# Kernel tuning notes

Hardware: AMD Instinct MI355X
Metric: run time of the kernel (lower is better)

Reference implementation:

```python
import jax, jax.numpy as jnp
import numpy as np

N, K, D, H, DK, DV, L, E = 16384, 16, 128, 8, 16, 16, 2, 32
DFF = 4 * D
EPS = 1e-5


def _ln(x, g, b):
    mu = jnp.mean(x, axis=-1, keepdims=True)
    var = jnp.var(x, axis=-1, keepdims=True)
    return (x - mu) * jax.lax.rsqrt(var + EPS) * g + b


def setup_inputs() -> dict:
    key = jax.random.key(0)
    ks = jax.random.split(key, 20)
    inp = {
        "node_h": jax.random.normal(ks[0], (N, D), jnp.float32),
        "src_idx": jax.random.randint(ks[1], (N, K), 0, N),
        "edge_feat": jax.random.normal(ks[2], (N, K, E), jnp.float32),
        "t": jax.random.uniform(ks[3], (N, K), jnp.float32),
        "t_now": jnp.ones((1,), jnp.float32),
        # params (linear weights stored [in, out])
        "edge_fc_w": jax.random.normal(ks[4], (E, D), jnp.float32) * (2.0 / (E + D)) ** 0.5,
        "edge_fc_b": jnp.zeros((D,), jnp.float32),
        "basis_freq": jnp.asarray(1.0 / 10 ** np.linspace(0, 9, D), jnp.float32),
        "phase": jax.random.normal(ks[5], (D,), jnp.float32),
        "wq": jax.random.normal(ks[6], (L, D, H * DK), jnp.float32) * np.sqrt(2.0 / (D + DK)),
        "wk": jax.random.normal(ks[7], (L, D, H * DK), jnp.float32) * np.sqrt(2.0 / (D + DK)),
        "wv": jax.random.normal(ks[8], (L, D, H * DV), jnp.float32) * np.sqrt(2.0 / (D + DV)),
        "attn_fc_w": jax.random.normal(ks[9], (L, H * DV, D), jnp.float32) * (2.0 / (H * DV + D)) ** 0.5,
        "attn_fc_b": jnp.zeros((L, D), jnp.float32),
        "attn_ln_g": jnp.ones((L, D), jnp.float32),
        "attn_ln_b": jnp.zeros((L, D), jnp.float32),
        "ffn_w1": jax.random.normal(ks[10], (L, D, DFF), jnp.float32) * (1.0 / D) ** 0.5,
        "ffn_b1": jnp.zeros((L, DFF), jnp.float32),
        "ffn_w2": jax.random.normal(ks[11], (L, DFF, D), jnp.float32) * (1.0 / DFF) ** 0.5,
        "ffn_b2": jnp.zeros((L, D), jnp.float32),
        "ffn_ln_g": jnp.ones((L, D), jnp.float32),
        "ffn_ln_b": jnp.zeros((L, D), jnp.float32),
        "fea2node_w": jax.random.normal(ks[12], (D, D), jnp.float32) * (2.0 / (D + D)) ** 0.5,
        "fea2node_b": jnp.zeros((D,), jnp.float32),
        "final_ln_g": jnp.ones((D,), jnp.float32),
        "final_ln_b": jnp.zeros((D,), jnp.float32),
    }
    return inp


def reference(node_h, src_idx, edge_feat, t, t_now,
              edge_fc_w, edge_fc_b, basis_freq, phase,
              wq, wk, wv, attn_fc_w, attn_fc_b, attn_ln_g, attn_ln_b,
              ffn_w1, ffn_b1, ffn_w2, ffn_b2, ffn_ln_g, ffn_ln_b,
              fea2node_w, fea2node_b, final_ln_g, final_ln_b):
    scale = 1.0 / np.sqrt(DK).astype(np.float32)
    # message_func: gather src features, edge transform, temporal encoding
    t_enc = jnp.cos((t_now[0] - t)[..., None] * basis_freq + phase)        # [N,K,D]
    z = node_h[src_idx] + jax.nn.gelu(edge_feat @ edge_fc_w + edge_fc_b) + t_enc
    # reduce_func: inner_layer transformer blocks over the K-neighbor mailbox
    f = z
    for i in range(L):
        q = (f @ wq[i]).reshape(N, K, H, DK)
        k = (f @ wk[i]).reshape(N, K, H, DK)
        v = (f @ wv[i]).reshape(N, K, H, DV)
        attn = jax.nn.softmax(jnp.einsum('nqhd,nkhd->nhqk', q, k) * scale, axis=-1)
        out = jnp.einsum('nhqk,nkhd->nqhd', attn, v).reshape(N, K, H * DV)
        f = _ln(out @ attn_fc_w[i] + attn_fc_b[i] + f, attn_ln_g[i], attn_ln_b[i])
        hid = jax.nn.relu(f @ ffn_w1[i] + ffn_b1[i])                        # [N,K,4D]
        f = _ln(hid @ ffn_w2[i] + ffn_b2[i] + f, ffn_ln_g[i], ffn_ln_b[i])
    pooled = jnp.mean(f, axis=1)                                            # [N,D]
    out = _ln(jax.nn.gelu(pooled @ fea2node_w + fea2node_b) + node_h,
              final_ln_g, final_ln_b)
    return out
```

## Files before the change

### kernel.cpp

```cpp
#include <hip/hip_runtime.h>

#define NN 16384
#define OFF_EWT 0
#define OFF_WQT 4096
#define OFF_WKT 36864
#define OFF_WVT 69632
#define OFF_AFT 102400
#define OFF_W1T 135168
#define OFF_W2T 266240
#define OFF_F2N 397312
#define TOTAL_W 413696
#define FB_BYTE_OFF (1 << 20)

typedef __attribute__((ext_vector_type(8))) short bf16x8;
typedef __attribute__((ext_vector_type(4))) short bf16x4;
typedef __attribute__((ext_vector_type(4))) float f32x4;

static __device__ __forceinline__ short f2bf(float f) {
  unsigned u = __builtin_bit_cast(unsigned, f);
  u += 0x7fffu + ((u >> 16) & 1u);
  return (short)(u >> 16);
}
static __device__ __forceinline__ float bf2f(short h) {
  unsigned u = ((unsigned)(unsigned short)h) << 16;
  return __builtin_bit_cast(float, u);
}
static __device__ __forceinline__ float gelu_f(float x) {
  float e = __expf(1.5957691216057308f * (x + 0.044715f * x * x * x));
  return x - x / (e + 1.0f);
}
static __device__ __forceinline__ f32x4 mfma16(bf16x8 a, bf16x8 b, f32x4 c) {
  return __builtin_amdgcn_mfma_f32_16x16x32_bf16(a, b, c, 0, 0, 0);
}
#define SWZM(row) (((((row) & 7) << 4)) ^ ((((row) >> 3) & 3) << 5))
static __device__ __forceinline__ int swzb(int row, int col) {
  return row * 256 + ((col * 2) ^ SWZM(row));
}
static __device__ __forceinline__ bf16x8 tile_ld8(const short* base, int row, int col) {
  return *(const bf16x8*)((const char*)base + swzb(row, col));
}
static __device__ __forceinline__ void tile_st16(short* base, int row, int col, short v) {
  *(short*)((char*)base + swzb(row, col)) = v;
}
static __device__ __forceinline__ float tile_ldf(const short* base, int row, int col) {
  return bf2f(*(const short*)((const char*)base + swzb(row, col)));
}
static __device__ __forceinline__ void gll16(const short* sp, void* dstb) {
  __builtin_amdgcn_global_load_lds(
      (const __attribute__((address_space(1))) unsigned int*)sp,
      (__attribute__((address_space(3))) unsigned int*)dstb, 16, 0, 0);
}
static __device__ __forceinline__ void stage_h8(short* dst, const short* src, int stride,
                                                int w, int lane) {
  #pragma unroll
  for (int it = 0; it < 2; ++it) {
    int dbase = (it * 8 + w) * 1024;
    int d = dbase + lane * 16;
    int row = d >> 8;
    int scolb = (d & 255) ^ SWZM(row);
    gll16(src + row * stride + (scolb >> 1), (char*)dst + dbase);
  }
}
static __device__ __forceinline__ void stage_full8(short* dst, const short* src, int stride,
                                                   int w, int lane) {
  #pragma unroll
  for (int it = 0; it < 4; ++it) {
    int dbase = (it * 8 + w) * 1024;
    int d = dbase + lane * 16;
    int row = d >> 8;
    int scolb = (d & 255) ^ SWZM(row);
    gll16(src + row * stride + (scolb >> 1), (char*)dst + dbase);
  }
}
static __device__ __forceinline__ void stage_f(short* dst, const short* src, int lane) {
  #pragma unroll
  for (int it = 0; it < 4; ++it) {
    int dbase = it * 1024;
    int d = dbase + lane * 16;
    int row = d >> 8;
    int scolb = (d & 255) ^ SWZM(row);
    gll16(src + row * 128 + (scolb >> 1), (char*)dst + dbase);
  }
}

#define LDS_FENCE() do {                                       \
    asm volatile("s_waitcnt lgkmcnt(0)" ::: "memory");         \
    __builtin_amdgcn_sched_barrier(0);                         \
  } while (0)

#define ENDSTEP() do {                                         \
    __syncthreads();                                           \
    short* _t = bc; bc = bn; bn = _t;                          \
  } while (0)

#define LD_FA(SRC)                                                        \
  _Pragma("unroll") for (int _s = 0; _s < 4; ++_s)                        \
      fA[_s] = tile_ld8((SRC), li, _s * 32 + lq * 8);

#define ST_TILE(T, ACC)                                                   \
  _Pragma("unroll") for (int _c = 0; _c < 8; ++_c)                        \
    _Pragma("unroll") for (int _r = 0; _r < 4; ++_r)                      \
      tile_st16((T), lq * 4 + _r, _c * 16 + li, f2bf((ACC)[_c][_r]));

#define PROJ4H(BB, RO)                                                    \
    f32x4 g0 = F0, g1 = F0, g2 = F0, g3 = F0;                             \
    _Pragma("unroll") for (int _s = 0; _s < 4; ++_s) {                    \
      int _sc = _s * 32 + lq * 8;                                         \
      g0 = mfma16(fA[_s], tile_ld8((BB), (RO) + 0 + li, _sc), g0);        \
      g1 = mfma16(fA[_s], tile_ld8((BB), (RO) + 16 + li, _sc), g1);       \
      g2 = mfma16(fA[_s], tile_ld8((BB), (RO) + 32 + li, _sc), g2);       \
      g3 = mfma16(fA[_s], tile_ld8((BB), (RO) + 48 + li, _sc), g3);       \
    }

#define ST4H(DST, HB)                                                     \
    _Pragma("unroll") for (int _r = 0; _r < 4; ++_r) {                    \
      tile_st16((DST), lq * 4 + _r, ((HB) * 4 + 0) * 16 + li, f2bf(g0[_r])); \
      tile_st16((DST), lq * 4 + _r, ((HB) * 4 + 1) * 16 + li, f2bf(g1[_r])); \
      tile_st16((DST), lq * 4 + _r, ((HB) * 4 + 2) * 16 + li, f2bf(g2[_r])); \
      tile_st16((DST), lq * 4 + _r, ((HB) * 4 + 3) * 16 + li, f2bf(g3[_r])); \
    }

#define ACC4H(AR, CB, BB, RO)                                             \
    _Pragma("unroll") for (int _s = 0; _s < 4; ++_s) {                    \
      int _sc = _s * 32 + lq * 8;                                         \
      acc[(CB) + 0] = mfma16(AR[_s], tile_ld8((BB), (RO) + 0 + li, _sc), acc[(CB) + 0]);  \
      acc[(CB) + 1] = mfma16(AR[_s], tile_ld8((BB), (RO) + 16 + li, _sc), acc[(CB) + 1]); \
      acc[(CB) + 2] = mfma16(AR[_s], tile_ld8((BB), (RO) + 32 + li, _sc), acc[(CB) + 2]); \
      acc[(CB) + 3] = mfma16(AR[_s], tile_ld8((BB), (RO) + 48 + li, _sc), acc[(CB) + 3]); \
    }

#define LAYER_NORM(A, GP, BP) do {                                        \
    float _gg[8], _bb[8];                                                 \
    _Pragma("unroll") for (int _c = 0; _c < 8; ++_c) {                    \
      _gg[_c] = (GP)[_c * 16 + li]; _bb[_c] = (BP)[_c * 16 + li]; }       \
    _Pragma("unroll") for (int _r = 0; _r < 4; ++_r) {                    \
      float _s1 = 0.f, _s2 = 0.f;                                         \
      _Pragma("unroll") for (int _c = 0; _c < 8; ++_c) {                  \
        float _v = (A)[_c][_r]; _s1 += _v; _s2 += _v * _v; }              \
      _Pragma("unroll") for (int _m = 1; _m <= 8; _m <<= 1) {             \
        _s1 += __shfl_xor(_s1, _m, 64); _s2 += __shfl_xor(_s2, _m, 64); } \
      float _mean = _s1 * (1.f / 128.f);                                  \
      float _var = _s2 * (1.f / 128.f) - _mean * _mean;                   \
      float _rstd = rsqrtf(_var + 1e-5f);                                 \
      _Pragma("unroll") for (int _c = 0; _c < 8; ++_c)                    \
        (A)[_c][_r] = ((A)[_c][_r] - _mean) * _rstd * _gg[_c] + _bb[_c];  \
    }                                                                     \
  } while (0)

#define ATTN(MYQ, MYK, VACC, OA) do {                                     \
    f32x4 _st[8];                                                         \
    _Pragma("unroll") for (int _h = 0; _h < 8; ++_h) {                    \
      bf16x8 _ka = B0, _qa = B0;                                          \
      if (lq < 2) {                                                       \
        _ka = tile_ld8((MYK), li, _h * 16 + lq * 8);                      \
        _qa = tile_ld8((MYQ), li, _h * 16 + lq * 8);                      \
      }                                                                   \
      _st[_h] = mfma16(_ka, _qa, F0);                                     \
    }                                                                     \
    LDS_FENCE();                                                          \
    _Pragma("unroll") for (int _c = 0; _c < 8; ++_c) {                    \
      bf16x4 _pk;                                                         \
      _Pragma("unroll") for (int _r = 0; _r < 4; ++_r)                    \
        _pk[_r] = f2bf((VACC)[_c][_r]);                                   \
      *(bf16x4*)((MYK) + (_c * 16 + li) * 16 + lq * 4) = _pk;             \
    }                                                                     \
    LDS_FENCE();                                                          \
    _Pragma("unroll") for (int _h = 0; _h < 8; ++_h) {                    \
      float _p[4]; float _mx = -1e30f;                                    \
      _Pragma("unroll") for (int _r = 0; _r < 4; ++_r) {                  \
        _p[_r] = _st[_h][_r] * 0.25f; _mx = fmaxf(_mx, _p[_r]); }         \
      _mx = fmaxf(_mx, __shfl_xor(_mx, 16, 64));                          \
      _mx = fmaxf(_mx, __shfl_xor(_mx, 32, 64));                          \
      float _sum = 0.f;                                                   \
      _Pragma("unroll") for (int _r = 0; _r < 4; ++_r) {                  \
        _p[_r] = __expf(_p[_r] - _mx); _sum += _p[_r]; }                  \
      _sum += __shfl_xor(_sum, 16, 64);                                   \
      _sum += __shfl_xor(_sum, 32, 64);                                   \
      float _inv = 1.0f / _sum;                                           \
      _Pragma("unroll") for (int _r = 0; _r < 4; ++_r) _p[_r] *= _inv;    \
      bf16x8 _pa;                                                         \
      _Pragma("unroll") for (int _j = 0; _j < 8; ++_j) {                  \
        float _v = __shfl(_p[_j & 3], li + 16 * (2 * lq + (_j >> 2)), 64);\
        _pa[_j] = (lq < 2) ? f2bf(_v) : (short)0;                         \
      }                                                                   \
      bf16x8 _vb = B0;                                                    \
      if (lq < 2) _vb = *(const bf16x8*)((MYK) + (_h * 16 + li) * 16 + lq * 8); \
      f32x4 _o = mfma16(_pa, _vb, F0);                                    \
      _Pragma("unroll") for (int _r = 0; _r < 4; ++_r)                    \
        tile_st16((MYQ), lq * 4 + _r, _h * 16 + li, f2bf(_o[_r]));        \
    }                                                                     \
    LDS_FENCE();                                                          \
    _Pragma("unroll") for (int _s = 0; _s < 4; ++_s)                      \
      (OA)[_s] = tile_ld8((MYQ), li, _s * 32 + lq * 8);                   \
  } while (0)

__global__ void prep_kernel(const float* __restrict__ ew, const float* __restrict__ wq,
                            const float* __restrict__ wk, const float* __restrict__ wv,
                            const float* __restrict__ afc, const float* __restrict__ w1,
                            const float* __restrict__ w2, const float* __restrict__ f2n,
                            short* __restrict__ wsb) {
  int tt = blockIdx.x * 256 + threadIdx.x;
  if (tt >= TOTAL_W) return;
  short v;
  if (tt < OFF_WQT) {
    int u = tt; int row = u >> 5, colr = u & 31;
    v = f2bf(ew[colr * 128 + row]);
  } else if (tt < OFF_WKT) {
    int u = tt - OFF_WQT; int i = u >> 14; u &= 16383; int row = u >> 7, colr = u & 127;
    v = f2bf(wq[i * 16384 + colr * 128 + row]);
  } else if (tt < OFF_WVT) {
    int u = tt - OFF_WKT; int i = u >> 14; u &= 16383; int row = u >> 7, colr = u & 127;
    v = f2bf(wk[i * 16384 + colr * 128 + row]);
  } else if (tt < OFF_AFT) {
    int u = tt - OFF_WVT; int i = u >> 14; u &= 16383; int row = u >> 7, colr = u & 127;
    v = f2bf(wv[i * 16384 + colr * 128 + row]);
  } else if (tt < OFF_W1T) {
    int u = tt - OFF_AFT; int i = u >> 14; u &= 16383; int row = u >> 7, colr = u & 127;
    v = f2bf(afc[i * 16384 + colr * 128 + row]);
  } else if (tt < OFF_W2T) {
    int u = tt - OFF_W1T; int i = u >> 16; u &= 65535; int row = u >> 7, colr = u & 127;
    v = f2bf(w1[i * 65536 + colr * 512 + row]);
  } else if (tt < OFF_F2N) {
    int u = tt - OFF_W2T; int i = u >> 16; u &= 65535; int row = u >> 9, colr = u & 511;
    v = f2bf(w2[i * 65536 + colr * 128 + row]);
  } else {
    int u = tt - OFF_F2N; int row = u >> 7, colr = u & 127;
    v = f2bf(f2n[colr * 128 + row]);
  }
  wsb[tt] = v;
}

__global__ __launch_bounds__(512, 2) void attn_kernel(
    const float* __restrict__ node_h, const int* __restrict__ src_idx,
    const float* __restrict__ edge_feat, const float* __restrict__ t_arr,
    const float* __restrict__ t_now, const float* __restrict__ edge_fc_b,
    const float* __restrict__ basis_freq, const float* __restrict__ phase,
    const float* __restrict__ attn_fc_b, const float* __restrict__ attn_ln_g,
    const float* __restrict__ attn_ln_b, const short* __restrict__ wsb,
    short* __restrict__ fbuf, int il, int do_msg) {
  __shared__ __align__(16) short bufs0[8192];
  __shared__ __align__(16) short bufs1[8192];
  __shared__ __align__(16) short qk[8][4096];

  const int tid = (int)threadIdx.x;
  const int w = tid >> 6, lane = tid & 63, li = lane & 15, lq = lane >> 4;
  const int n = (int)blockIdx.x * 8 + w;
  short* myQ = qk[w];
  short* myK = qk[w] + 2048;
  short* bc = bufs0;
  short* bn = bufs1;
  const f32x4 F0 = {0.f, 0.f, 0.f, 0.f};
  const bf16x8 B0 = {0, 0, 0, 0, 0, 0, 0, 0};
  const short* WQT = wsb + OFF_WQT + il * 16384;
  const short* WKT = wsb + OFF_WKT + il * 16384;
  const short* WVT = wsb + OFF_WVT + il * 16384;
  const short* AFT = wsb + OFF_AFT + il * 16384;

  stage_h8(bc, WQT, 128, w, lane);

  f32x4 acc[8];
  if (do_msg) {
    const float tnow = t_now[0];
    {
      const float* ef = edge_feat + ((size_t)(n * 16 + li)) * 32 + lq * 8;
      f32x4 e0 = *(const f32x4*)(ef);
      f32x4 e1 = *(const f32x4*)(ef + 4);
      bf16x8 ea;
      #pragma unroll
      for (int j = 0; j < 4; ++j) { ea[j] = f2bf(e0[j]); ea[j + 4] = f2bf(e1[j]); }
      const short* ewt = wsb + OFF_EWT;
      #pragma unroll
      for (int c = 0; c < 8; ++c) {
        bf16x8 eb = *(const bf16x8*)(ewt + (c * 16 + li) * 32 + lq * 8);
        acc[c] = mfma16(ea, eb, F0);
      }
    }
    {
      float bfq[8], phs[8], ebs[8];
      #pragma unroll
      for (int c = 0; c < 8; ++c) {
        int col = c * 16 + li;
        bfq[c] = basis_freq[col]; phs[c] = phase[col]; ebs[c] = edge_fc_b[col];
      }
      #pragma unroll
      for (int r = 0; r < 4; ++r) {
        int m = lq * 4 + r;
        int sidx = src_idx[n * 16 + m];
        float dt = tnow - t_arr[n * 16 + m];
        const float* nh = node_h + (size_t)sidx * 128;
        #pragma unroll
        for (int c = 0; c < 8; ++c) {
          int col = c * 16 + li;
          float x = gelu_f(acc[c][r] + ebs[c]);
          x += nh[col];
          x += __cosf(dt * bfq[c] + phs[c]);
          acc[c][r] = x;
        }
      }
    }
    ST_TILE(myQ, acc);
  } else {
    stage_f(myQ, fbuf + (size_t)n * 2048, lane);
  }
  __syncthreads();
  if (!do_msg) {
    #pragma unroll
    for (int c = 0; c < 8; ++c)
      #pragma unroll
      for (int r = 0; r < 4; ++r)
        acc[c][r] = tile_ldf(myQ, lq * 4 + r, c * 16 + li);
  }

  bf16x8 fA[4], oa_[4];

  #pragma unroll
  for (int h = 0; h < 2; ++h) {
    const short* nx = (h == 0) ? (WQT + 8192) : WKT;
    stage_h8(bn, nx, 128, w, lane);
    if (h == 0) LD_FA(myQ);
    { PROJ4H(bc, 0); ST4H(myQ, h); }
    ENDSTEP();
  }
  #pragma unroll
  for (int h = 0; h < 2; ++h) {
    const short* nx = (h == 0) ? (WKT + 8192) : WVT;
    stage_h8(bn, nx, 128, w, lane);
    { PROJ4H(bc, 0); ST4H(myK, h); }
    ENDSTEP();
  }
  {
    f32x4 vacc[8];
    #pragma unroll
    for (int h = 0; h < 2; ++h) {
      const short* nx = (h == 0) ? (WVT + 8192) : AFT;
      stage_h8(bn, nx, 128, w, lane);
      {
        PROJ4H(bc, 0);
        vacc[h * 4 + 0] = g0; vacc[h * 4 + 1] = g1;
        vacc[h * 4 + 2] = g2; vacc[h * 4 + 3] = g3;
      }
      if (h == 1) {
        LDS_FENCE();
        ATTN(myQ, myK, vacc, oa_);
      }
      ENDSTEP();
    }
  }
  #pragma unroll
  for (int h = 0; h < 2; ++h) {
    if (h == 0) stage_h8(bn, AFT + 8192, 128, w, lane);
    #pragma unroll
    for (int j = 0; j < 4; ++j) {
      float b = attn_fc_b[il * 128 + (h * 4 + j) * 16 + li];
      #pragma unroll
      for (int r = 0; r < 4; ++r) acc[h * 4 + j][r] += b;
    }
    ACC4H(oa_, h * 4, bc, 0);
    if (h == 1) {
      LAYER_NORM(acc, attn_ln_g + il * 128, attn_ln_b + il * 128);
      ST_TILE(myQ, acc);
    }
    ENDSTEP();
  }
  LDS_FENCE();
  #pragma unroll
  for (int j = 0; j < 4; ++j) {
    int row = lane >> 2, colb = (lane & 3) * 32 + j * 8;
    bf16x8 v = tile_ld8(myQ, row, colb);
    *(bf16x8*)(fbuf + (size_t)n * 2048 + row * 128 + colb) = v;
  }
}

__global__ __launch_bounds__(512, 2) void ffn_kernel(
    const float* __restrict__ ffn_b1, const float* __restrict__ ffn_b2,
    const float* __restrict__ ffn_ln_g, const float* __restrict__ ffn_ln_b,
    const float* __restrict__ f2n_b, const float* __restrict__ fin_g,
    const float* __restrict__ fin_b, const float* __restrict__ node_h,
    const short* __restrict__ wsb, short* __restrict__ fbuf,
    float* __restrict__ out, int il, int last) {
  __shared__ __align__(16) short bufs0[16384];
  __shared__ __align__(16) short bufs1[16384];
  __shared__ __align__(16) short qk[8][2048];

  const int tid = (int)threadIdx.x;
  const int w = tid >> 6, lane = tid & 63, li = lane & 15, lq = lane >> 4;
  const int n = (int)blockIdx.x * 8 + w;
  short* myK = qk[w];
  short* bc = bufs0;
  short* bn = bufs1;
  const f32x4 F0 = {0.f, 0.f, 0.f, 0.f};
  const short* W1T = wsb + OFF_W1T + il * 65536;
  const short* W2T = wsb + OFF_W2T + il * 65536;

  stage_full8(bc, W1T, 128, w, lane);
  stage_f(myK, fbuf + (size_t)n * 2048, lane);
  __syncthreads();

  bf16x8 fA[4], ha_[4];
  LD_FA(myK);
  f32x4 acc[8];
  #pragma unroll
  for (int c = 0; c < 8; ++c) {
    float b2 = ffn_b2[il * 128 + c * 16 + li];
    #pragma unroll
    for (int r = 0; r < 4; ++r)
      acc[c][r] = tile_ldf(myK, lq * 4 + r, c * 16 + li) + b2;
  }
  LDS_FENCE();

  for (int ct = 0; ct < 4; ++ct) {
    const short* W1c = W1T + ct * 16384;
    const short* W2c = W2T + ct * 128;
    const float* b1p = ffn_b1 + il * 512 + ct * 128;
    stage_full8(bn, W2c, 512, w, lane);
    #pragma unroll
    for (int h = 0; h < 2; ++h) {
      PROJ4H(bc, h * 64);
      #pragma unroll
      for (int j = 0; j < 4; ++j) {
        float b1 = b1p[(h * 4 + j) * 16 + li];
        f32x4 gx = j == 0 ? g0 : j == 1 ? g1 : j == 2 ? g2 : g3;
        #pragma unroll
        for (int r = 0; r < 4; ++r)
          tile_st16(myK, lq * 4 + r, (h * 4 + j) * 16 + li, f2bf(fmaxf(gx[r] + b1, 0.f)));
      }
    }
    LDS_FENCE();
    #pragma unroll
    for (int s = 0; s < 4; ++s) ha_[s] = tile_ld8(myK, li, s * 32 + lq * 8);
    ENDSTEP();
    if (ct < 3) stage_full8(bn, W1T + (ct + 1) * 16384, 128, w, lane);
    ACC4H(ha_, 0, bc, 0);
    ACC4H(ha_, 4, bc, 64);
    if (ct == 3)
      LAYER_NORM(acc, ffn_ln_g + il * 128, ffn_ln_b + il * 128);
    ENDSTEP();
  }

  if (last) {
    float pc[8];
    #pragma unroll
    for (int c = 0; c < 8; ++c) {
      float s = acc[c][0] + acc[c][1] + acc[c][2] + acc[c][3];
      s += __shfl_xor(s, 16, 64);
      s += __shfl_xor(s, 32, 64);
      pc[c] = s * (1.f / 16.f);
    }
    float* ps = (float*)myK;
    if (lq == 0) {
      #pragma unroll
      for (int c = 0; c < 8; ++c) ps[c * 16 + li] = pc[c];
    }
    LDS_FENCE();
    const short* F2NT = wsb + OFF_F2N;
    float yv[2];
    #pragma unroll
    for (int half = 0; half < 2; ++half) {
      int col = half * 64 + lane;
      float dot = 0.f;
      for (int d0 = 0; d0 < 128; d0 += 8) {
        bf16x8 wv8 = *(const bf16x8*)(F2NT + col * 128 + d0);
        f32x4 p0 = *(const f32x4*)(ps + d0);
        f32x4 p1 = *(const f32x4*)(ps + d0 + 4);
        dot += p0[0] * bf2f(wv8[0]) + p0[1] * bf2f(wv8[1]) + p0[2] * bf2f(wv8[2]) + p0[3] * bf2f(wv8[3]);
        dot += p1[0] * bf2f(wv8[4]) + p1[1] * bf2f(wv8[5]) + p1[2] * bf2f(wv8[6]) + p1[3] * bf2f(wv8[7]);
      }
      yv[half] = gelu_f(dot + f2n_b[col]) + node_h[(size_t)n * 128 + col];
    }
    float s1 = yv[0] + yv[1], s2 = yv[0] * yv[0] + yv[1] * yv[1];
    #pragma unroll
    for (int m = 1; m <= 32; m <<= 1) { s1 += __shfl_xor(s1, m, 64); s2 += __shfl_xor(s2, m, 64); }
    float mean = s1 * (1.f / 128.f);
    float var = s2 * (1.f / 128.f) - mean * mean;
    float rstd = rsqrtf(var + 1e-5f);
    #pragma unroll
    for (int half = 0; half < 2; ++half) {
      int col = half * 64 + lane;
      out[(size_t)n * 128 + col] = (yv[half] - mean) * rstd * fin_g[col] + fin_b[col];
    }
  } else {
    ST_TILE(myK, acc);
    LDS_FENCE();
    #pragma unroll
    for (int j = 0; j < 4; ++j) {
      int row = lane >> 2, colb = (lane & 3) * 32 + j * 8;
      bf16x8 v = tile_ld8(myK, row, colb);
      *(bf16x8*)(fbuf + (size_t)n * 2048 + row * 128 + colb) = v;
    }
  }
}

extern "C" void kernel_launch(void* const* d_in, const int* in_sizes, int n_in,
                              void* d_out, int out_size, void* d_ws, size_t ws_size,
                              hipStream_t stream) {
  const float* node_h    = (const float*)d_in[0];
  const int*   src_idx   = (const int*)d_in[1];
  const float* edge_feat = (const float*)d_in[2];
  const float* t_arr     = (const float*)d_in[3];
  const float* t_now     = (const float*)d_in[4];
  const float* edge_fc_w = (const float*)d_in[5];
  const float* edge_fc_b = (const float*)d_in[6];
  const float* basis_frq = (const float*)d_in[7];
  const float* phase     = (const float*)d_in[8];
  const float* wq        = (const float*)d_in[9];
  const float* wk        = (const float*)d_in[10];
  const float* wv        = (const float*)d_in[11];
  const float* attn_fc_w = (const float*)d_in[12];
  const float* attn_fc_b = (const float*)d_in[13];
  const float* attn_ln_g = (const float*)d_in[14];
  const float* attn_ln_b = (const float*)d_in[15];
  const float* ffn_w1    = (const float*)d_in[16];
  const float* ffn_b1    = (const float*)d_in[17];
  const float* ffn_w2    = (const float*)d_in[18];
  const float* ffn_b2    = (const float*)d_in[19];
  const float* ffn_ln_g  = (const float*)d_in[20];
  const float* ffn_ln_b  = (const float*)d_in[21];
  const float* f2n_w     = (const float*)d_in[22];
  const float* f2n_b     = (const float*)d_in[23];
  const float* fin_g     = (const float*)d_in[24];
  const float* fin_b     = (const float*)d_in[25];
  short* wsb  = (short*)d_ws;
  short* fbuf = (short*)((char*)d_ws + FB_BYTE_OFF);

  prep_kernel<<<(TOTAL_W + 255) / 256, 256, 0, stream>>>(
      edge_fc_w, wq, wk, wv, attn_fc_w, ffn_w1, ffn_w2, f2n_w, wsb);
  attn_kernel<<<NN / 8, 512, 0, stream>>>(
      node_h, src_idx, edge_feat, t_arr, t_now, edge_fc_b, basis_frq, phase,
      attn_fc_b, attn_ln_g, attn_ln_b, wsb, fbuf, 0, 1);
  ffn_kernel<<<NN / 8, 512, 0, stream>>>(
      ffn_b1, ffn_b2, ffn_ln_g, ffn_ln_b, f2n_b, fin_g, fin_b, node_h,
      wsb, fbuf, (float*)d_out, 0, 0);
  attn_kernel<<<NN / 8, 512, 0, stream>>>(
      node_h, src_idx, edge_feat, t_arr, t_now, edge_fc_b, basis_frq, phase,
      attn_fc_b, attn_ln_g, attn_ln_b, wsb, fbuf, 1, 0);
  ffn_kernel<<<NN / 8, 512, 0, stream>>>(
      ffn_b1, ffn_b2, ffn_ln_g, ffn_ln_b, f2n_b, fin_g, fin_b, node_h,
      wsb, fbuf, (float*)d_out, 1, 1);
}
```

Before: 635.5 us.

## Process two nodes per wave in FFN kernel to reuse weight-tile loads

The FFN kernel now uses 4 waves per block, each handling two nodes, so every B-fragment read from LDS feeds two MFMAs instead of one. Weight staging shrinks to 64-row half-tiles with finer-grained double buffering, which halves LDS per buffer. Register pressure roughly doubles (two accumulator sets of 8 tiles plus two A-fragment sets), and the launch bound drops to 256 threads with min 1 block per SM. Occupancy and latency hiding may suffer as a result.

```diff
diff --git a/kernel.cpp b/kernel.cpp
--- a/kernel.cpp
+++ b/kernel.cpp
@@ -61,11 +61,11 @@
     gll16(src + row * stride + (scolb >> 1), (char*)dst + dbase);
   }
 }
-static __device__ __forceinline__ void stage_full8(short* dst, const short* src, int stride,
-                                                   int w, int lane) {
+static __device__ __forceinline__ void stage_h4(short* dst, const short* src, int stride,
+                                                int w, int lane) {
   #pragma unroll
   for (int it = 0; it < 4; ++it) {
-    int dbase = (it * 8 + w) * 1024;
+    int dbase = (it * 4 + w) * 1024;
     int d = dbase + lane * 16;
     int row = d >> 8;
     int scolb = (d & 255) ^ SWZM(row);
@@ -127,6 +127,38 @@
       acc[(CB) + 1] = mfma16(AR[_s], tile_ld8((BB), (RO) + 16 + li, _sc), acc[(CB) + 1]); \
       acc[(CB) + 2] = mfma16(AR[_s], tile_ld8((BB), (RO) + 32 + li, _sc), acc[(CB) + 2]); \
       acc[(CB) + 3] = mfma16(AR[_s], tile_ld8((BB), (RO) + 48 + li, _sc), acc[(CB) + 3]); \
+    }
+
+#define PROJ2H(BB)                                                        \
+    f32x4 ga0 = F0, ga1 = F0, ga2 = F0, ga3 = F0;                         \
+    f32x4 gb0 = F0, gb1 = F0, gb2 = F0, gb3 = F0;                         \
+    _Pragma("unroll") for (int _s = 0; _s < 4; ++_s) {                    \
+      int _sc = _s * 32 + lq * 8;                                         \
+      bf16x8 _b0 = tile_ld8((BB), 0 + li, _sc);                           \
+      bf16x8 _b1 = tile_ld8((BB), 16 + li, _sc);                          \
+      bf16x8 _b2 = tile_ld8((BB), 32 + li, _sc);                          \
+      bf16x8 _b3 = tile_ld8((BB), 48 + li, _sc);                          \
+      ga0 = mfma16(fA0[_s], _b0, ga0); gb0 = mfma16(fA1[_s], _b0, gb0);   \
+      ga1 = mfma16(fA0[_s], _b1, ga1); gb1 = mfma16(fA1[_s], _b1, gb1);   \
+      ga2 = mfma16(fA0[_s], _b2, ga2); gb2 = mfma16(fA1[_s], _b2, gb2);   \
+      ga3 = mfma16(fA0[_s], _b3, ga3); gb3 = mfma16(fA1[_s], _b3, gb3);   \
+    }
+
+#define ACC2H(AR0, AR1, CB, BB)                                           \
+    _Pragma("unroll") for (int _s = 0; _s < 4; ++_s) {                    \
+      int _sc = _s * 32 + lq * 8;                                         \
+      bf16x8 _b0 = tile_ld8((BB), 0 + li, _sc);                           \
+      bf16x8 _b1 = tile_ld8((BB), 16 + li, _sc);                          \
+      bf16x8 _b2 = tile_ld8((BB), 32 + li, _sc);                          \
+      bf16x8 _b3 = tile_ld8((BB), 48 + li, _sc);                          \
+      acc0[(CB) + 0] = mfma16(AR0[_s], _b0, acc0[(CB) + 0]);              \
+      acc1[(CB) + 0] = mfma16(AR1[_s], _b0, acc1[(CB) + 0]);              \
+      acc0[(CB) + 1] = mfma16(AR0[_s], _b1, acc0[(CB) + 1]);              \
+      acc1[(CB) + 1] = mfma16(AR1[_s], _b1, acc1[(CB) + 1]);              \
+      acc0[(CB) + 2] = mfma16(AR0[_s], _b2, acc0[(CB) + 2]);              \
+      acc1[(CB) + 2] = mfma16(AR1[_s], _b2, acc1[(CB) + 2]);              \
+      acc0[(CB) + 3] = mfma16(AR0[_s], _b3, acc0[(CB) + 3]);              \
+      acc1[(CB) + 3] = mfma16(AR1[_s], _b3, acc1[(CB) + 3]);              \
     }
 
 #define LAYER_NORM(A, GP, BP) do {                                        \
@@ -371,40 +403,48 @@
   }
 }
 
-__global__ __launch_bounds__(512, 2) void ffn_kernel(
+__global__ __launch_bounds__(256, 1) void ffn_kernel(
     const float* __restrict__ ffn_b1, const float* __restrict__ ffn_b2,
     const float* __restrict__ ffn_ln_g, const float* __restrict__ ffn_ln_b,
     const float* __restrict__ f2n_b, const float* __restrict__ fin_g,
     const float* __restrict__ fin_b, const float* __restrict__ node_h,
     const short* __restrict__ wsb, short* __restrict__ fbuf,
     float* __restrict__ out, int il, int last) {
-  __shared__ __align__(16) short bufs0[16384];
-  __shared__ __align__(16) short bufs1[16384];
-  __shared__ __align__(16) short qk[8][2048];
+  __shared__ __align__(16) short bufs0[8192];
+  __shared__ __align__(16) short bufs1[8192];
+  __shared__ __align__(16) short tiles[4][4096];
 
   const int tid = (int)threadIdx.x;
   const int w = tid >> 6, lane = tid & 63, li = lane & 15, lq = lane >> 4;
-  const int n = (int)blockIdx.x * 8 + w;
-  short* myK = qk[w];
+  const int n0 = (int)blockIdx.x * 8 + w * 2, n1 = n0 + 1;
+  short* t0 = tiles[w];
+  short* t1 = tiles[w] + 2048;
   short* bc = bufs0;
   short* bn = bufs1;
   const f32x4 F0 = {0.f, 0.f, 0.f, 0.f};
   const short* W1T = wsb + OFF_W1T + il * 65536;
   const short* W2T = wsb + OFF_W2T + il * 65536;
 
-  stage_full8(bc, W1T, 128, w, lane);
-  stage_f(myK, fbuf + (size_t)n * 2048, lane);
+  stage_h4(bc, W1T, 128, w, lane);
+  stage_f(t0, fbuf + (size_t)n0 * 2048, lane);
+  stage_f(t1, fbuf + (size_t)n1 * 2048, lane);
   __syncthreads();
 
-  bf16x8 fA[4], ha_[4];
-  LD_FA(myK);
-  f32x4 acc[8];
+  bf16x8 fA0[4], fA1[4], ha0_[4], ha1_[4];
+  #pragma unroll
+  for (int s = 0; s < 4; ++s) {
+    fA0[s] = tile_ld8(t0, li, s * 32 + lq * 8);
+    fA1[s] = tile_ld8(t1, li, s * 32 + lq * 8);
+  }
+  f32x4 acc0[8], acc1[8];
   #pragma unroll
   for (int c = 0; c < 8; ++c) {
     float b2 = ffn_b2[il * 128 + c * 16 + li];
     #pragma unroll
-    for (int r = 0; r < 4; ++r)
-      acc[c][r] = tile_ldf(myK, lq * 4 + r, c * 16 + li) + b2;
+    for (int r = 0; r < 4; ++r) {
+      acc0[c][r] = tile_ldf(t0, lq * 4 + r, c * 16 + li) + b2;
+      acc1[c][r] = tile_ldf(t1, lq * 4 + r, c * 16 + li) + b2;
+    }
   }
   LDS_FENCE();
 
@@ -412,80 +452,112 @@
     const short* W1c = W1T + ct * 16384;
     const short* W2c = W2T + ct * 128;
     const float* b1p = ffn_b1 + il * 512 + ct * 128;
-    stage_full8(bn, W2c, 512, w, lane);
     #pragma unroll
     for (int h = 0; h < 2; ++h) {
-      PROJ4H(bc, h * 64);
-      #pragma unroll
-      for (int j = 0; j < 4; ++j) {
-        float b1 = b1p[(h * 4 + j) * 16 + li];
-        f32x4 gx = j == 0 ? g0 : j == 1 ? g1 : j == 2 ? g2 : g3;
+      const short* nx = (h == 0) ? (W1c + 64 * 128) : W2c;
+      stage_h4(bn, nx, (h == 0) ? 128 : 512, w, lane);
+      {
+        PROJ2H(bc);
+        float b1v[4];
         #pragma unroll
-        for (int r = 0; r < 4; ++r)
-          tile_st16(myK, lq * 4 + r, (h * 4 + j) * 16 + li, f2bf(fmaxf(gx[r] + b1, 0.f)));
-      }
-    }
-    LDS_FENCE();
-    #pragma unroll
-    for (int s = 0; s < 4; ++s) ha_[s] = tile_ld8(myK, li, s * 32 + lq * 8);
-    ENDSTEP();
-    if (ct < 3) stage_full8(bn, W1T + (ct + 1) * 16384, 128, w, lane);
-    ACC4H(ha_, 0, bc, 0);
-    ACC4H(ha_, 4, bc, 64);
-    if (ct == 3)
-      LAYER_NORM(acc, ffn_ln_g + il * 128, ffn_ln_b + il * 128);
-    ENDSTEP();
+        for (int j = 0; j < 4; ++j) b1v[j] = b1p[(h * 4 + j) * 16 + li];
+        #pragma unroll
+        for (int r = 0; r < 4; ++r) {
+          tile_st16(t0, lq * 4 + r, (h * 4 + 0) * 16 + li, f2bf(fmaxf(ga0[r] + b1v[0], 0.f)));
+          tile_st16(t0, lq * 4 + r, (h * 4 + 1) * 16 + li, f2bf(fmaxf(ga1[r] + b1v[1], 0.f)));
+          tile_st16(t0, lq * 4 + r, (h * 4 + 2) * 16 + li, f2bf(fmaxf(ga2[r] + b1v[2], 0.f)));
+          tile_st16(t0, lq * 4 + r, (h * 4 + 3) * 16 + li, f2bf(fmaxf(ga3[r] + b1v[3], 0.f)));
+          tile_st16(t1, lq * 4 + r, (h * 4 + 0) * 16 + li, f2bf(fmaxf(gb0[r] + b1v[0], 0.f)));
+          tile_st16(t1, lq * 4 + r, (h * 4 + 1) * 16 + li, f2bf(fmaxf(gb1[r] + b1v[1], 0.f)));
+          tile_st16(t1, lq * 4 + r, (h * 4 + 2) * 16 + li, f2bf(fmaxf(gb2[r] + b1v[2], 0.f)));
+          tile_st16(t1, lq * 4 + r, (h * 4 + 3) * 16 + li, f2bf(fmaxf(gb3[r] + b1v[3], 0.f)));
+        }
+      }
+      if (h == 1) {
+        LDS_FENCE();
+        #pragma unroll
+        for (int s = 0; s < 4; ++s) {
+          ha0_[s] = tile_ld8(t0, li, s * 32 + lq * 8);
+          ha1_[s] = tile_ld8(t1, li, s * 32 + lq * 8);
+        }
+      }
+      ENDSTEP();
+    }
+    #pragma unroll
+    for (int h = 0; h < 2; ++h) {
+      if (h == 0) stage_h4(bn, W2c + 64 * 512, 512, w, lane);
+      else if (ct < 3) stage_h4(bn, W1T + (ct + 1) * 16384, 128, w, lane);
+      ACC2H(ha0_, ha1_, h * 4, bc);
+      if (ct == 3 && h == 1) {
+        LAYER_NORM(acc0, ffn_ln_g + il * 128, ffn_ln_b + il * 128);
+        LAYER_NORM(acc1, ffn_ln_g + il * 128, ffn_ln_b + il * 128);
+      }
+      ENDSTEP();
+    }
   }
 
   if (last) {
-    float pc[8];
+    float pc0[8], pc1[8];
     #pragma unroll
     for (int c = 0; c < 8; ++c) {
-      float s = acc[c][0] + acc[c][1] + acc[c][2] + acc[c][3];
-      s += __shfl_xor(s, 16, 64);
-      s += __shfl_xor(s, 32, 64);
-      pc[c] = s * (1.f / 16.f);
-    }
-    float* ps = (float*)myK;
+      float s0 = acc0[c][0] + acc0[c][1] + acc0[c][2] + acc0[c][3];
+      float s1 = acc1[c][0] + acc1[c][1] + acc1[c][2] + acc1[c][3];
+      s0 += __shfl_xor(s0, 16, 64); s0 += __shfl_xor(s0, 32, 64);
+      s1 += __shfl_xor(s1, 16, 64); s1 += __shfl_xor(s1, 32, 64);
+      pc0[c] = s0 * (1.f / 16.f);
+      pc1[c] = s1 * (1.f / 16.f);
+    }
+    float* ps0 = (float*)t0;
+    float* ps1 = (float*)t1;
     if (lq == 0) {
       #pragma unroll
-      for (int c = 0; c < 8; ++c) ps[c * 16 + li] = pc[c];
+      for (int c = 0; c < 8; ++c) { ps0[c * 16 + li] = pc0[c]; ps1[c * 16 + li] = pc1[c]; }
     }
     LDS_FENCE();
     const short* F2NT = wsb + OFF_F2N;
-    float yv[2];
-    #pragma unroll
-    for (int half = 0; half < 2; ++half) {
-      int col = half * 64 + lane;
-      float dot = 0.f;
-      for (int d0 = 0; d0 < 128; d0 += 8) {
-        bf16x8 wv8 = *(const bf16x8*)(F2NT + col * 128 + d0);
-        f32x4 p0 = *(const f32x4*)(ps + d0);
-        f32x4 p1 = *(const f32x4*)(ps + d0 + 4);
-        dot += p0[0] * bf2f(wv8[0]) + p0[1] * bf2f(wv8[1]) + p0[2] * bf2f(wv8[2]) + p0[3] * bf2f(wv8[3]);
-        dot += p1[0] * bf2f(wv8[4]) + p1[1] * bf2f(wv8[5]) + p1[2] * bf2f(wv8[6]) + p1[3] * bf2f(wv8[7]);
-      }
-      yv[half] = gelu_f(dot + f2n_b[col]) + node_h[(size_t)n * 128 + col];
-    }
-    float s1 = yv[0] + yv[1], s2 = yv[0] * yv[0] + yv[1] * yv[1];
-    #pragma unroll
-    for (int m = 1; m <= 32; m <<= 1) { s1 += __shfl_xor(s1, m, 64); s2 += __shfl_xor(s2, m, 64); }
-    float mean = s1 * (1.f / 128.f);
-    float var = s2 * (1.f / 128.f) - mean * mean;
-    float rstd = rsqrtf(var + 1e-5f);
-    #pragma unroll
-    for (int half = 0; half < 2; ++half) {
-      int col = half * 64 + lane;
-      out[(size_t)n * 128 + col] = (yv[half] - mean) * rstd * fin_g[col] + fin_b[col];
+    #pragma unroll
+    for (int nd = 0; nd < 2; ++nd) {
+      const float* ps = nd ? ps1 : ps0;
+      int n = nd ? n1 : n0;
+      float yv[2];
+      #pragma unroll
+      for (int half = 0; half < 2; ++half) {
+        int col = half * 64 + lane;
+        float dot = 0.f;
+        for (int d0 = 0; d0 < 128; d0 += 8) {
+          bf16x8 wv8 = *(const bf16x8*)(F2NT + col * 128 + d0);
+          f32x4 p0 = *(const f32x4*)(ps + d0);
+          f32x4 p1 = *(const f32x4*)(ps + d0 + 4);
+          dot += p0[0] * bf2f(wv8[0]) + p0[1] * bf2f(wv8[1]) + p0[2] * bf2f(wv8[2]) + p0[3] * bf2f(wv8[3]);
+          dot += p1[0] * bf2f(wv8[4]) + p1[1] * bf2f(wv8[5]) + p1[2] * bf2f(wv8[6]) + p1[3] * bf2f(wv8[7]);
+        }
+        yv[half] = gelu_f(dot + f2n_b[col]) + node_h[(size_t)n * 128 + col];
+      }
+      float s1v = yv[0] + yv[1], s2v = yv[0] * yv[0] + yv[1] * yv[1];
+      #pragma unroll
+      for (int m = 1; m <= 32; m <<= 1) {
+        s1v += __shfl_xor(s1v, m, 64); s2v += __shfl_xor(s2v, m, 64);
+      }
+      float mean = s1v * (1.f / 128.f);
+      float var = s2v * (1.f / 128.f) - mean * mean;
+      float rstd = rsqrtf(var + 1e-5f);
+      #pragma unroll
+      for (int half = 0; half < 2; ++half) {
+        int col = half * 64 + lane;
+        out[(size_t)n * 128 + col] = (yv[half] - mean) * rstd * fin_g[col] + fin_b[col];
+      }
     }
   } else {
-    ST_TILE(myK, acc);
+    ST_TILE(t0, acc0);
+    ST_TILE(t1, acc1);
     LDS_FENCE();
     #pragma unroll
     for (int j = 0; j < 4; ++j) {
       int row = lane >> 2, colb = (lane & 3) * 32 + j * 8;
-      bf16x8 v = tile_ld8(myK, row, colb);
-      *(bf16x8*)(fbuf + (size_t)n * 2048 + row * 128 + colb) = v;
+      bf16x8 v0 = tile_ld8(t0, row, colb);
+      bf16x8 v1 = tile_ld8(t1, row, colb);
+      *(bf16x8*)(fbuf + (size_t)n0 * 2048 + row * 128 + colb) = v0;
+      *(bf16x8*)(fbuf + (size_t)n1 * 2048 + row * 128 + colb) = v1;
     }
   }
 }
@@ -527,13 +599,13 @@
   attn_kernel<<<NN / 8, 512, 0, stream>>>(
       node_h, src_idx, edge_feat, t_arr, t_now, edge_fc_b, basis_frq, phase,
       attn_fc_b, attn_ln_g, attn_ln_b, wsb, fbuf, 0, 1);
-  ffn_kernel<<<NN / 8, 512, 0, stream>>>(
+  ffn_kernel<<<NN / 8, 256, 0, stream>>>(
       ffn_b1, ffn_b2, ffn_ln_g, ffn_ln_b, f2n_b, fin_g, fin_b, node_h,
       wsb, fbuf, (float*)d_out, 0, 0);
   attn_kernel<<<NN / 8, 512, 0, stream>>>(
       node_h, src_idx, edge_feat, t_arr, t_now, edge_fc_b, basis_frq, phase,
       attn_fc_b, attn_ln_g, attn_ln_b, wsb, fbuf, 1, 0);
-  ffn_kernel<<<NN / 8, 512, 0, stream>>>(
+  ffn_kernel<<<NN / 8, 256, 0, stream>>>(
       ffn_b1, ffn_b2, ffn_ln_g, ffn_ln_b, f2n_b, fin_g, fin_b, node_h,
       wsb, fbuf, (float*)d_out, 1, 1);
 }
```

Measured after the change: 691.3 us. +8.8%, slower.
